# Optimization experiments

Measured on AMD Instinct MI355X. Metric: run time of the kernel, lower is better.

Reference implementation:

```python
import jax, jax.numpy as jnp
import numpy as np

B, T, DIM, E, H = 128, 512, 256, 512, 512

def _linear_params(key, out_dim, in_dim, bias=True):
    k1, k2 = jax.random.split(key)
    bound = 1.0 / np.sqrt(in_dim)
    W = jax.random.uniform(k1, (out_dim, in_dim), jnp.float32, -bound, bound)
    if bias:
        b = jax.random.uniform(k2, (out_dim,), jnp.float32, -bound, bound)
        return W, b
    return W

def setup_inputs() -> dict:
    key = jax.random.key(0)
    ks = jax.random.split(key, 12)
    x_t = jax.random.normal(ks[0], (B, T, DIM), jnp.float32)
    h0 = jax.random.normal(ks[1], (B, H), jnp.float32)
    c0 = jax.random.normal(ks[2], (B, H), jnp.float32)
    We, be = _linear_params(ks[3], E, DIM)
    Wf, bf = _linear_params(ks[4], H, E)   # forget input proj
    Wi, bi = _linear_params(ks[5], H, E)   # input gate
    Wg, bg = _linear_params(ks[6], H, E)   # cell candidate
    Wo, bo = _linear_params(ks[7], H, E)   # output gate
    Rf = _linear_params(ks[8], H, H, bias=False)
    Ri = _linear_params(ks[9], H, H, bias=False)
    Rg = _linear_params(ks[10], H, H, bias=False)
    Ro = _linear_params(ks[11], H, H, bias=False)
    return dict(x_t=x_t, h0=h0, c0=c0, We=We, be=be,
                Wf=Wf, bf=bf, Wi=Wi, bi=bi, Wg=Wg, bg=bg, Wo=Wo, bo=bo,
                Rf=Rf, Ri=Ri, Rg=Rg, Ro=Ro)

def reference(x_t, h0, c0, We, be, Wf, bf, Wi, bi, Wg, bg, Wo, bo, Rf, Ri, Rg, Ro):
    # Embedding: [B,T,DIM] -> [B,T,E]
    xe = jnp.einsum('btd,ed->bte', x_t, We) + be
    # Batch all input-to-hidden projections across time in one GEMM each.
    xf = jnp.einsum('bte,he->bth', xe, Wf) + bf
    xi = jnp.einsum('bte,he->bth', xe, Wi) + bi
    xg = jnp.einsum('bte,he->bth', xe, Wg) + bg
    xo = jnp.einsum('bte,he->bth', xe, Wo) + bo
    xs = jnp.stack([xi, xf, xg, xo], axis=0)  # [4,B,T,H]

    def step(carry, x4):
        h, c = carry
        xi_t, xf_t, xg_t, xo_t = x4
        i = jax.nn.sigmoid(xi_t + h @ Ri.T)
        f = jax.nn.sigmoid(xf_t + h @ Rf.T)
        g = jnp.tanh(xg_t + h @ Rg.T)
        c_next = g * i + f * c
        o = jax.nn.sigmoid(xo_t + h @ Ro.T)
        h_next = o * jnp.tanh(c_next)
        return (h_next, c_next), h_next

    (h_last, c_last), hs = jax.lax.scan(step, (h0, c0), jnp.moveaxis(xs, 2, 0))
    hidden_seq = jnp.swapaxes(hs, 0, 1)  # [B,T,H]
    return hidden_seq, h_last, c_last
```

## Files before the change

### kernel.cpp

```cpp
#include <hip/hip_runtime.h>
#include <hip/hip_bf16.h>

#define B_ 128
#define T_ 512
#define DIM_ 256
#define E_ 512
#define H_ 512
#define NB_ 32
#define NG_ 8
#define WROW 1032
#define FSTRIDE 32

typedef __attribute__((ext_vector_type(8))) short short8;
typedef __attribute__((ext_vector_type(4))) float floatx4;
typedef unsigned long long ull_t;

__device__ __forceinline__ float sigmoidf_(float x) {
  return __fdividef(1.0f, 1.0f + __expf(-x));
}

__device__ __forceinline__ float tanhf_(float x) {
  x = fminf(15.0f, fmaxf(-15.0f, x));
  const float e = __expf(2.0f * x);
  return __fdividef(e - 1.0f, e + 1.0f);
}

__device__ __forceinline__ short f2bs(float f) {
  __hip_bfloat16 h = __float2bfloat16(f);
  return *reinterpret_cast<short*>(&h);
}

__global__ __launch_bounds__(256) void cvt_we(const float* __restrict__ src,
                                              __hip_bfloat16* __restrict__ dst,
                                              int n) {
  int i = blockIdx.x * 256 + threadIdx.x;
  if (i < n) dst[i] = __float2bfloat16(src[i]);
}

__global__ __launch_bounds__(256) void embed_gemm(
    const float* __restrict__ A,
    const __hip_bfloat16* __restrict__ W,
    const float* __restrict__ bias,
    __hip_bfloat16* __restrict__ C)
{
  const int tid = threadIdx.x;
  const int lane = tid & 63;
  const int w = tid >> 6;
  const int q = lane >> 4;
  const int l15 = lane & 15;
  const int m0 = blockIdx.x * 32 + (w >> 1) * 16;
  const int n0 = (w & 1) * 256;

  const float* a_base = A + (size_t)(m0 + l15) * DIM_ + q * 8;

  floatx4 acc[16];
#pragma unroll
  for (int j = 0; j < 16; ++j) acc[j] = (floatx4){0.f, 0.f, 0.f, 0.f};

  for (int ks = 0; ks < 8; ++ks) {
    const float* ap = a_base + ks * 32;
    short8 a;
#pragma unroll
    for (int j = 0; j < 8; ++j) a[j] = f2bs(ap[j]);
    short8 bf[16];
#pragma unroll
    for (int j = 0; j < 16; ++j) {
      const short* b_ptr =
          (const short*)W + (n0 + j * 16 + l15) * DIM_ + ks * 32 + q * 8;
      bf[j] = *(const short8*)b_ptr;
    }
#pragma unroll
    for (int j = 0; j < 16; ++j)
      acc[j] = __builtin_amdgcn_mfma_f32_16x16x32_bf16(a, bf[j], acc[j], 0, 0, 0);
  }

#pragma unroll
  for (int j = 0; j < 16; ++j) {
    const int col = n0 + j * 16 + l15;
    const float bv = bias[col];
#pragma unroll
    for (int r = 0; r < 4; ++r) {
      const int row = m0 + q * 4 + r;
      C[(size_t)row * E_ + col] = __float2bfloat16(acc[j][r] + bv);
    }
  }
}

__global__ __launch_bounds__(256, 1) void lstm_persist(
    const float* __restrict__ h0,
    const float* __restrict__ c0,
    const float* __restrict__ Wi_, const float* __restrict__ bi_,
    const float* __restrict__ Wf_, const float* __restrict__ bf_,
    const float* __restrict__ Wg_, const float* __restrict__ bg_,
    const float* __restrict__ Wo_, const float* __restrict__ bo_,
    const float* __restrict__ Ri_, const float* __restrict__ Rf_,
    const float* __restrict__ Rg_, const float* __restrict__ Ro_,
    const __hip_bfloat16* __restrict__ xe,
    unsigned* __restrict__ hbuf32,
    unsigned* __restrict__ flags,
    float* __restrict__ out)
{
  extern __shared__ short wts[];
  __shared__ float pbuf[4][4][16][17];
  __shared__ float cbuf[16][16];
  __shared__ float bias_s[4][16];

  const int tid = threadIdx.x;
  const int lane = tid & 63;
  const int w = tid >> 6;
  const int q = lane >> 4;
  const int l15 = lane & 15;
  const int blk = blockIdx.x;
  const int g = blk & 7;
  const int jb = blk >> 3;
  const int b0 = g * 16;
  const int d0 = jb * 16;
  unsigned* flags_g = flags + g * (NB_ * FSTRIDE);
  ull_t* hbuf64 = (ull_t*)hbuf32;

  const float* Wp[4] = {Wi_, Wf_, Wg_, Wo_};
  const float* Rp[4] = {Ri_, Rf_, Rg_, Ro_};
  const float* bp[4] = {bi_, bf_, bg_, bo_};

  for (int idx = tid; idx < 64 * 128; idx += 256) {
    const int row = idx >> 7;
    const int ch = idx & 127;
    const int G = row >> 4, dl = row & 15;
    const int k = ch * 8;
    const float* src = (k < 512) ? Wp[G] + (d0 + dl) * E_ + k
                                 : Rp[G] + (d0 + dl) * H_ + (k - 512);
    short8 v;
#pragma unroll
    for (int s = 0; s < 8; ++s) v[s] = f2bs(src[s]);
    *(short8*)&wts[row * WROW + k] = v;
  }
  if (tid < 64) {
    const int G = tid >> 4, n = tid & 15;
    bias_s[G][n] = bp[G][d0 + n];
  }
  {
    const int m = tid >> 4, n = tid & 15;
    cbuf[m][n] = c0[(b0 + m) * H_ + d0 + n];
  }
  if (tid < 128) {
    const int u = g * 4096 + jb * 128 + tid;
    unsigned pk = (unsigned)(unsigned short)f2bs(h0[2 * u]) |
                  ((unsigned)(unsigned short)f2bs(h0[2 * u + 1]) << 16);
    __hip_atomic_store(&hbuf32[u], pk, __ATOMIC_RELAXED,
                       __HIP_MEMORY_SCOPE_AGENT);
  }

  __syncthreads();
  if (tid == 0)
    __hip_atomic_store(&flags_g[jb * FSTRIDE], 1u, __ATOMIC_RELAXED,
                       __HIP_MEMORY_SCOPE_AGENT);

  const short* xbase = (const short*)xe +
      (size_t)(b0 + l15) * T_ * E_ + w * 256 + q * 8;
  const int lds_base = l15 * WROW + w * 256 + q * 8;

  short8 cur[8];
  if (w < 2) {
#pragma unroll
    for (int s = 0; s < 8; ++s) cur[s] = *(const short8*)(xbase + s * 32);
  }

  if (w == 3) {
    unsigned* fp = &flags_g[(lane & 31) * FSTRIDE];
    for (;;) {
      unsigned v = __hip_atomic_load(fp, __ATOMIC_RELAXED,
                                     __HIP_MEMORY_SCOPE_AGENT);
      if (__all((int)(v >= 1u))) break;
    }
  }
  __syncthreads();

  float hval = 0.f, cv = 0.f;
  const int m = tid >> 4, n = tid & 15;

  for (int t = 0; t < T_; ++t) {
    if (t > 0)
      out[((size_t)(b0 + m) * T_ + (t - 1)) * H_ + d0 + n] = hval;

    if (w >= 2) {
      const ull_t* hb = hbuf64 + (size_t)(t & 1) * (B_ * H_ / 4) +
                        (b0 + l15) * (H_ / 4) + (w - 2) * 64 + q * 2;
#pragma unroll
      for (int s = 0; s < 8; ++s) {
        union { ull_t u[2]; short8 v8; } uu;
        uu.u[0] = __hip_atomic_load(hb + s * 8, __ATOMIC_RELAXED,
                                    __HIP_MEMORY_SCOPE_AGENT);
        uu.u[1] = __hip_atomic_load(hb + s * 8 + 1, __ATOMIC_RELAXED,
                                    __HIP_MEMORY_SCOPE_AGENT);
        cur[s] = uu.v8;
      }
    }

    floatx4 acc[4];
#pragma unroll
    for (int G = 0; G < 4; ++G) acc[G] = (floatx4){0.f, 0.f, 0.f, 0.f};
#pragma unroll
    for (int s = 0; s < 8; ++s)
#pragma unroll
      for (int G = 0; G < 4; ++G) {
        short8 bfr = *(const short8*)&wts[G * 16 * WROW + lds_base + s * 32];
        acc[G] = __builtin_amdgcn_mfma_f32_16x16x32_bf16(cur[s], bfr, acc[G], 0, 0, 0);
      }

    if (w < 2 && t + 1 < T_) {
      const short* xp = xbase + (size_t)(t + 1) * E_;
#pragma unroll
      for (int s = 0; s < 8; ++s) cur[s] = *(const short8*)(xp + s * 32);
    }

#pragma unroll
    for (int G = 0; G < 4; ++G)
#pragma unroll
      for (int r = 0; r < 4; ++r)
        pbuf[w][G][q * 4 + r][l15] = acc[G][r];
    __syncthreads();

    float pre[4];
#pragma unroll
    for (int G = 0; G < 4; ++G)
      pre[G] = pbuf[0][G][m][n] + pbuf[1][G][m][n] + pbuf[2][G][m][n] +
               pbuf[3][G][m][n] + bias_s[G][n];
    const float iv = sigmoidf_(pre[0]);
    const float fv = sigmoidf_(pre[1]);
    const float gv = tanhf_(pre[2]);
    const float ov = sigmoidf_(pre[3]);
    cv = gv * iv + fv * cbuf[m][n];
    cbuf[m][n] = cv;
    hval = ov * tanhf_(cv);

    if (t + 1 < T_) {
      unsigned hv = (unsigned)(unsigned short)f2bs(hval);
      unsigned ov2 = __shfl_xor(hv, 1);
      if ((n & 1) == 0) {
        unsigned pk = hv | (ov2 << 16);
        __hip_atomic_store(
            &hbuf32[((t + 1) & 1) * (B_ * H_ / 2) + (b0 + m) * (H_ / 2) +
                    ((d0 + n) >> 1)],
            pk, __ATOMIC_RELAXED, __HIP_MEMORY_SCOPE_AGENT);
      }
      __syncthreads();
      if (tid == 0)
        __hip_atomic_store(&flags_g[jb * FSTRIDE], (unsigned)(t + 2),
                           __ATOMIC_RELAXED, __HIP_MEMORY_SCOPE_AGENT);
      if (w == 3) {
        unsigned* fp = &flags_g[(lane & 31) * FSTRIDE];
        const unsigned tgt = (unsigned)(t + 2);
        for (;;) {
          unsigned v = __hip_atomic_load(fp, __ATOMIC_RELAXED,
                                         __HIP_MEMORY_SCOPE_AGENT);
          if (__all((int)(v >= tgt))) break;
        }
      }
      __syncthreads();
    }
  }

  out[((size_t)(b0 + m) * T_ + (T_ - 1)) * H_ + d0 + n] = hval;
  out[(size_t)B_ * T_ * H_ + (b0 + m) * H_ + d0 + n] = hval;
  out[(size_t)B_ * T_ * H_ + B_ * H_ + (b0 + m) * H_ + d0 + n] = cv;
}

extern "C" void kernel_launch(void* const* d_in, const int* in_sizes, int n_in,
                              void* d_out, int out_size, void* d_ws,
                              size_t ws_size, hipStream_t stream) {
  const float* x_t = (const float*)d_in[0];
  const float* h0  = (const float*)d_in[1];
  const float* c0  = (const float*)d_in[2];
  const float* We  = (const float*)d_in[3];
  const float* be  = (const float*)d_in[4];
  const float* Wf  = (const float*)d_in[5];
  const float* bf_ = (const float*)d_in[6];
  const float* Wi  = (const float*)d_in[7];
  const float* bi  = (const float*)d_in[8];
  const float* Wg  = (const float*)d_in[9];
  const float* bg  = (const float*)d_in[10];
  const float* Wo  = (const float*)d_in[11];
  const float* bo  = (const float*)d_in[12];
  const float* Rf  = (const float*)d_in[13];
  const float* Ri  = (const float*)d_in[14];
  const float* Rg  = (const float*)d_in[15];
  const float* Ro  = (const float*)d_in[16];
  float* out = (float*)d_out;

  char* ws = (char*)d_ws;
  unsigned* flags = (unsigned*)ws;
  unsigned* hbuf  = (unsigned*)(ws + 32768);
  __hip_bfloat16* Web = (__hip_bfloat16*)(ws + 32768 + 262144);
  __hip_bfloat16* xe  = (__hip_bfloat16*)(ws + 32768 + 2 * 262144);

  hipMemsetAsync(flags, 0, 32768, stream);

  cvt_we<<<(E_ * DIM_ + 255) / 256, 256, 0, stream>>>(We, Web, E_ * DIM_);

  embed_gemm<<<(B_ * T_) / 32, 256, 0, stream>>>(x_t, Web, be, xe);

  const size_t lds_bytes = 64 * WROW * sizeof(short);
  lstm_persist<<<NG_ * NB_, 256, lds_bytes, stream>>>(
      h0, c0, Wi, bi, Wf, bf_, Wg, bg, Wo, bo, Ri, Rf, Rg, Ro, xe, hbuf, flags,
      out);
}
```

Before: 2.035 ms.

## Replace flag barriers with per-timestep sentinel-valued hidden-state slots

Drops the per-group flag counters and spin barriers. Each timestep now gets its own hidden-state slot, pre-filled with 0xFF sentinels. Consumer waves poll the data itself and issue MFMAs for each 16-byte chunk as soon as it is no longer the sentinel, so the two syncthreads and the flag store/poll per step go away and the recurrent matmul overlaps with arrival. The cost is a roughly 67 MB memset every call and a much larger workspace. Correctness relies on no real bf16 pair ever equalling 0xFFFFFFFF (that pattern is a NaN) and on the relaxed ordering behaving as intended.

```diff
diff --git a/kernel.cpp b/kernel.cpp
--- a/kernel.cpp
+++ b/kernel.cpp
@@ -9,7 +9,9 @@
 #define NB_ 32
 #define NG_ 8
 #define WROW 1032
-#define FSTRIDE 32
+#define SLOT32 (B_ * H_ / 2)
+#define SLOT64 (B_ * H_ / 4)
+#define NSLOT (T_ + 1)
 
 typedef __attribute__((ext_vector_type(8))) short short8;
 typedef __attribute__((ext_vector_type(4))) float floatx4;
@@ -97,11 +99,10 @@
     const float* __restrict__ Rg_, const float* __restrict__ Ro_,
     const __hip_bfloat16* __restrict__ xe,
     unsigned* __restrict__ hbuf32,
-    unsigned* __restrict__ flags,
     float* __restrict__ out)
 {
   extern __shared__ short wts[];
-  __shared__ float pbuf[4][4][16][17];
+  __shared__ float pbuf[4][4][16][16];
   __shared__ float cbuf[16][16];
   __shared__ float bias_s[4][16];
 
@@ -115,7 +116,6 @@
   const int jb = blk >> 3;
   const int b0 = g * 16;
   const int d0 = jb * 16;
-  unsigned* flags_g = flags + g * (NB_ * FSTRIDE);
   ull_t* hbuf64 = (ull_t*)hbuf32;
 
   const float* Wp[4] = {Wi_, Wf_, Wg_, Wo_};
@@ -151,9 +151,6 @@
   }
 
   __syncthreads();
-  if (tid == 0)
-    __hip_atomic_store(&flags_g[jb * FSTRIDE], 1u, __ATOMIC_RELAXED,
-                       __HIP_MEMORY_SCOPE_AGENT);
 
   const short* xbase = (const short*)xe +
       (size_t)(b0 + l15) * T_ * E_ + w * 256 + q * 8;
@@ -165,52 +162,66 @@
     for (int s = 0; s < 8; ++s) cur[s] = *(const short8*)(xbase + s * 32);
   }
 
-  if (w == 3) {
-    unsigned* fp = &flags_g[(lane & 31) * FSTRIDE];
-    for (;;) {
-      unsigned v = __hip_atomic_load(fp, __ATOMIC_RELAXED,
-                                     __HIP_MEMORY_SCOPE_AGENT);
-      if (__all((int)(v >= 1u))) break;
-    }
-  }
-  __syncthreads();
-
-  float hval = 0.f, cv = 0.f;
   const int m = tid >> 4, n = tid & 15;
 
   for (int t = 0; t < T_; ++t) {
-    if (t > 0)
-      out[((size_t)(b0 + m) * T_ + (t - 1)) * H_ + d0 + n] = hval;
+    floatx4 acc[4];
+#pragma unroll
+    for (int G = 0; G < 4; ++G) acc[G] = (floatx4){0.f, 0.f, 0.f, 0.f};
 
     if (w >= 2) {
-      const ull_t* hb = hbuf64 + (size_t)(t & 1) * (B_ * H_ / 4) +
+      const ull_t* hb = hbuf64 + (size_t)t * SLOT64 +
                         (b0 + l15) * (H_ / 4) + (w - 2) * 64 + q * 2;
-#pragma unroll
-      for (int s = 0; s < 8; ++s) {
-        union { ull_t u[2]; short8 v8; } uu;
-        uu.u[0] = __hip_atomic_load(hb + s * 8, __ATOMIC_RELAXED,
-                                    __HIP_MEMORY_SCOPE_AGENT);
-        uu.u[1] = __hip_atomic_load(hb + s * 8 + 1, __ATOMIC_RELAXED,
-                                    __HIP_MEMORY_SCOPE_AGENT);
-        cur[s] = uu.v8;
+      unsigned miss = 0xFFu;
+      ull_t ta[8], tb[8];
+      while (miss) {
+#pragma unroll
+        for (int s = 0; s < 8; ++s)
+          if (miss & (1u << s)) {
+            ta[s] = __hip_atomic_load(hb + s * 8, __ATOMIC_RELAXED,
+                                      __HIP_MEMORY_SCOPE_AGENT);
+            tb[s] = __hip_atomic_load(hb + s * 8 + 1, __ATOMIC_RELAXED,
+                                      __HIP_MEMORY_SCOPE_AGENT);
+          }
+#pragma unroll
+        for (int s = 0; s < 8; ++s)
+          if (miss & (1u << s)) {
+            const unsigned a0 = (unsigned)ta[s];
+            const unsigned a1 = (unsigned)(ta[s] >> 32);
+            const unsigned c0_ = (unsigned)tb[s];
+            const unsigned c1 = (unsigned)(tb[s] >> 32);
+            const bool fresh =
+                (a0 != 0xFFFFFFFFu) & (a1 != 0xFFFFFFFFu) &
+                (c0_ != 0xFFFFFFFFu) & (c1 != 0xFFFFFFFFu);
+            if (__all((int)fresh)) {
+              union { ull_t u[2]; short8 v8; } uu;
+              uu.u[0] = ta[s];
+              uu.u[1] = tb[s];
+#pragma unroll
+              for (int G = 0; G < 4; ++G) {
+                short8 bfr =
+                    *(const short8*)&wts[G * 16 * WROW + lds_base + s * 32];
+                acc[G] = __builtin_amdgcn_mfma_f32_16x16x32_bf16(uu.v8, bfr,
+                                                                 acc[G], 0, 0, 0);
+              }
+              miss &= ~(1u << s);
+            }
+          }
       }
-    }
-
-    floatx4 acc[4];
-#pragma unroll
-    for (int G = 0; G < 4; ++G) acc[G] = (floatx4){0.f, 0.f, 0.f, 0.f};
-#pragma unroll
-    for (int s = 0; s < 8; ++s)
-#pragma unroll
-      for (int G = 0; G < 4; ++G) {
-        short8 bfr = *(const short8*)&wts[G * 16 * WROW + lds_base + s * 32];
-        acc[G] = __builtin_amdgcn_mfma_f32_16x16x32_bf16(cur[s], bfr, acc[G], 0, 0, 0);
+    } else {
+#pragma unroll
+      for (int s = 0; s < 8; ++s)
+#pragma unroll
+        for (int G = 0; G < 4; ++G) {
+          short8 bfr = *(const short8*)&wts[G * 16 * WROW + lds_base + s * 32];
+          acc[G] = __builtin_amdgcn_mfma_f32_16x16x32_bf16(cur[s], bfr, acc[G],
+                                                           0, 0, 0);
+        }
+      if (t + 1 < T_) {
+        const short* xp = xbase + (size_t)(t + 1) * E_;
+#pragma unroll
+        for (int s = 0; s < 8; ++s) cur[s] = *(const short8*)(xp + s * 32);
       }
-
-    if (w < 2 && t + 1 < T_) {
-      const short* xp = xbase + (size_t)(t + 1) * E_;
-#pragma unroll
-      for (int s = 0; s < 8; ++s) cur[s] = *(const short8*)(xp + s * 32);
     }
 
 #pragma unroll
@@ -229,40 +240,30 @@
     const float fv = sigmoidf_(pre[1]);
     const float gv = tanhf_(pre[2]);
     const float ov = sigmoidf_(pre[3]);
-    cv = gv * iv + fv * cbuf[m][n];
+    const float cv = gv * iv + fv * cbuf[m][n];
     cbuf[m][n] = cv;
-    hval = ov * tanhf_(cv);
-
-    if (t + 1 < T_) {
+    const float hval = ov * tanhf_(cv);
+
+    {
       unsigned hv = (unsigned)(unsigned short)f2bs(hval);
       unsigned ov2 = __shfl_xor(hv, 1);
       if ((n & 1) == 0) {
         unsigned pk = hv | (ov2 << 16);
         __hip_atomic_store(
-            &hbuf32[((t + 1) & 1) * (B_ * H_ / 2) + (b0 + m) * (H_ / 2) +
+            &hbuf32[(size_t)(t + 1) * SLOT32 + (b0 + m) * (H_ / 2) +
                     ((d0 + n) >> 1)],
             pk, __ATOMIC_RELAXED, __HIP_MEMORY_SCOPE_AGENT);
       }
-      __syncthreads();
-      if (tid == 0)
-        __hip_atomic_store(&flags_g[jb * FSTRIDE], (unsigned)(t + 2),
-                           __ATOMIC_RELAXED, __HIP_MEMORY_SCOPE_AGENT);
-      if (w == 3) {
-        unsigned* fp = &flags_g[(lane & 31) * FSTRIDE];
-        const unsigned tgt = (unsigned)(t + 2);
-        for (;;) {
-          unsigned v = __hip_atomic_load(fp, __ATOMIC_RELAXED,
-                                         __HIP_MEMORY_SCOPE_AGENT);
-          if (__all((int)(v >= tgt))) break;
-        }
-      }
-      __syncthreads();
-    }
-  }
-
-  out[((size_t)(b0 + m) * T_ + (T_ - 1)) * H_ + d0 + n] = hval;
-  out[(size_t)B_ * T_ * H_ + (b0 + m) * H_ + d0 + n] = hval;
-  out[(size_t)B_ * T_ * H_ + B_ * H_ + (b0 + m) * H_ + d0 + n] = cv;
+    }
+
+    out[((size_t)(b0 + m) * T_ + t) * H_ + d0 + n] = hval;
+    if (t == T_ - 1) {
+      out[(size_t)B_ * T_ * H_ + (b0 + m) * H_ + d0 + n] = hval;
+      out[(size_t)B_ * T_ * H_ + B_ * H_ + (b0 + m) * H_ + d0 + n] = cv;
+    }
+
+    __syncthreads();
+  }
 }
 
 extern "C" void kernel_launch(void* const* d_in, const int* in_sizes, int n_in,
@@ -287,13 +288,13 @@
   const float* Ro  = (const float*)d_in[16];
   float* out = (float*)d_out;
 
+  const size_t HBUF_BYTES = (size_t)NSLOT * SLOT32 * 4;
   char* ws = (char*)d_ws;
-  unsigned* flags = (unsigned*)ws;
-  unsigned* hbuf  = (unsigned*)(ws + 32768);
-  __hip_bfloat16* Web = (__hip_bfloat16*)(ws + 32768 + 262144);
-  __hip_bfloat16* xe  = (__hip_bfloat16*)(ws + 32768 + 2 * 262144);
-
-  hipMemsetAsync(flags, 0, 32768, stream);
+  unsigned* hbuf = (unsigned*)ws;
+  __hip_bfloat16* Web = (__hip_bfloat16*)(ws + 67240960);
+  __hip_bfloat16* xe  = (__hip_bfloat16*)(ws + 67240960 + 262144);
+
+  hipMemsetAsync(hbuf, 0xFF, HBUF_BYTES, stream);
 
   cvt_we<<<(E_ * DIM_ + 255) / 256, 256, 0, stream>>>(We, Web, E_ * DIM_);
 
@@ -301,6 +302,5 @@
 
   const size_t lds_bytes = 64 * WROW * sizeof(short);
   lstm_persist<<<NG_ * NB_, 256, lds_bytes, stream>>>(
-      h0, c0, Wi, bi, Wf, bf_, Wg, bg, Wo, bo, Ri, Rf, Rg, Ro, xe, hbuf, flags,
-      out);
-}
+      h0, c0, Wi, bi, Wf, bf_, Wg, bg, Wo, bo, Ri, Rf, Rg, Ro, xe, hbuf, out);
+}
```

After: 2.937 ms. 44.3% more time.
